# Optimization experiments

Hardware: AMD Instinct MI355X
Metric: run time of the kernel (lower is better)

## Reference

```python
import jax, jax.numpy as jnp
import numpy as np

B, S, E = 2, 2048, 1024
H, BLK = 16, 32
HD = E // H


def setup_inputs() -> dict:
    key = jax.random.key(0)
    ks = jax.random.split(key, 9)
    s = 1.0 / np.sqrt(E)
    return {
        "x": jax.random.normal(ks[0], (B, S, E), dtype=jnp.float32),
        "Wq": jax.random.normal(ks[1], (E, E), dtype=jnp.float32) * s,
        "bq": jnp.zeros((E,), dtype=jnp.float32),
        "Wk": jax.random.normal(ks[2], (E, E), dtype=jnp.float32) * s,
        "bk": jnp.zeros((E,), dtype=jnp.float32),
        "Wv": jax.random.normal(ks[3], (E, E), dtype=jnp.float32) * s,
        "bv": jnp.zeros((E,), dtype=jnp.float32),
        "Wo": jax.random.normal(ks[4], (E, E), dtype=jnp.float32) * s,
        "bo": jnp.zeros((E,), dtype=jnp.float32),
    }


def reference(x, Wq, bq, Wk, bk, Wv, bv, Wo, bo):
    b, s, e = x.shape
    # projections (torch Linear: x @ W.T + b), split heads -> [b, h, s, hd]
    def proj(W, bias):
        return (x @ W.T + bias).reshape(b, s, H, HD).transpose(0, 2, 1, 3)

    q = proj(Wq, bq)
    k = proj(Wk, bk)
    v = proj(Wv, bv)

    scale = 1.0 / np.sqrt(HD)
    scores = jnp.einsum("bhqd,bhkd->bhqk", q, k) * scale  # [b,h,s,s]

    # block-causal mask: query block i attends to all key blocks j <= i
    idx = jnp.arange(s)
    allowed = (idx[None, :] // BLK) <= (idx[:, None] // BLK)  # [s, s]
    scores = jnp.where(allowed[None, None], scores, jnp.float32(-1e9))

    probs = jax.nn.softmax(scores, axis=-1)
    attn = jnp.einsum("bhqk,bhkd->bhqd", probs, v)  # [b,h,s,hd]
    out = attn.transpose(0, 2, 1, 3).reshape(b, s, e)
    return out @ Wo.T + bo
```

## Files before the change

kernel.cpp:

```cpp
#include <hip/hip_runtime.h>
#include <hip/hip_bf16.h>
#include <stdint.h>

#define BATCH 2
#define S_LEN 2048
#define EMB   1024
#define NHEAD 16
#define HDIM  64

typedef __attribute__((ext_vector_type(8)))  __bf16 bf16x8;
typedef __attribute__((ext_vector_type(4)))  __bf16 bf16x4;
typedef __attribute__((ext_vector_type(4)))  float  f32x4;
typedef __attribute__((ext_vector_type(16))) float  f32x16;

#define ZERO16 ((f32x16){0.f,0.f,0.f,0.f,0.f,0.f,0.f,0.f,0.f,0.f,0.f,0.f,0.f,0.f,0.f,0.f})
#define SM_SCALE_LOG2 0.18033688011112042f

static __device__ __forceinline__ void gload_lds16(const void* g, void* l) {
    __builtin_amdgcn_global_load_lds(
        (__attribute__((address_space(1))) void*)g,
        (__attribute__((address_space(3))) void*)l,
        16, 0, 0);
}

__global__ void f2b_all(const float* __restrict__ x,
                        const float* __restrict__ Wq, const float* __restrict__ Wk,
                        const float* __restrict__ Wv, const float* __restrict__ Wo,
                        __bf16* __restrict__ xb,
                        __bf16* __restrict__ wqb, __bf16* __restrict__ wkb,
                        __bf16* __restrict__ wvb, __bf16* __restrict__ wob) {
    int i = blockIdx.x * blockDim.x + threadIdx.x;
    const float* s;
    __bf16* d;
    int off;
    if (i < (1 << 20)) {
        s = x; d = xb; off = i;
    } else {
        int r   = i - (1 << 20);
        int seg = r >> 18;
        off = r & ((1 << 18) - 1);
        s = seg == 0 ? Wq : seg == 1 ? Wk : seg == 2 ? Wv : Wo;
        d = seg == 0 ? wqb : seg == 1 ? wkb : seg == 2 ? wvb : wob;
    }
    float4 v = reinterpret_cast<const float4*>(s)[off];
    bf16x4 o = { (__bf16)v.x, (__bf16)v.y, (__bf16)v.z, (__bf16)v.w };
    reinterpret_cast<bf16x4*>(d)[off] = o;
}

__global__ __launch_bounds__(256)
void gemm_o64(const __bf16* __restrict__ A, const __bf16* __restrict__ W,
              const float* __restrict__ bias, float* __restrict__ out,
              int M, int N, int K) {
    __shared__ __align__(16) __bf16 As[2][128 * 64];
    __shared__ __align__(16) __bf16 Bs[2][64 * 64];

    const int t    = threadIdx.x;
    const int w    = t >> 6;
    const int lane = t & 63;
    const int m0   = blockIdx.y * 128;
    const int n0   = blockIdx.x * 64;
    const int wr   = w * 32;
    const int fr   = lane & 15;
    const int g16  = lane >> 4;

    f32x4 acc[2][4];
#pragma unroll
    for (int i = 0; i < 2; ++i)
#pragma unroll
        for (int n = 0; n < 4; ++n) acc[i][n] = (f32x4){0.f, 0.f, 0.f, 0.f};

    auto stage = [&](int kt, int buf) {
#pragma unroll
        for (int i = 0; i < 4; ++i) {
            int chunk = i * 256 + t;
            int row   = chunk >> 3;
            int col   = ((chunk & 7) ^ (row & 7)) * 8;
            gload_lds16(A + (size_t)(m0 + row) * K + kt + col,
                        (char*)&As[buf][0] + i * 4096 + w * 1024);
        }
#pragma unroll
        for (int i = 0; i < 2; ++i) {
            int chunk = i * 256 + t;
            int row   = chunk >> 3;
            int col   = ((chunk & 7) ^ (row & 7)) * 8;
            gload_lds16(W + (size_t)(n0 + row) * K + kt + col,
                        (char*)&Bs[buf][0] + i * 4096 + w * 1024);
        }
    };

    stage(0, 0);
    __syncthreads();

    const int NK = K / 64;
    for (int k6 = 0; k6 < NK; ++k6) {
        const int cur = k6 & 1;
        if (k6 + 1 < NK) stage((k6 + 1) * 64, cur ^ 1);

#pragma unroll
        for (int kh = 0; kh < 2; ++kh) {
            bf16x8 af[2], bfv[4];
#pragma unroll
            for (int m = 0; m < 2; ++m) {
                int row = wr + m * 16 + fr;
                int cg  = ((4 * kh + g16) ^ (row & 7)) * 8;
                af[m] = *(const bf16x8*)&As[cur][row * 64 + cg];
            }
#pragma unroll
            for (int n = 0; n < 4; ++n) {
                int row = n * 16 + fr;
                int cg  = ((4 * kh + g16) ^ (row & 7)) * 8;
                bfv[n] = *(const bf16x8*)&Bs[cur][row * 64 + cg];
            }
#pragma unroll
            for (int m = 0; m < 2; ++m)
#pragma unroll
                for (int n = 0; n < 4; ++n)
                    acc[m][n] = __builtin_amdgcn_mfma_f32_16x16x32_bf16(
                        af[m], bfv[n], acc[m][n], 0, 0, 0);
        }
        __syncthreads();
    }

    const int rbase = (lane >> 4) * 4;
#pragma unroll
    for (int m = 0; m < 2; ++m) {
#pragma unroll
        for (int n = 0; n < 4; ++n) {
            int col  = n0 + n * 16 + fr;
            float bv = bias[col];
#pragma unroll
            for (int jj = 0; jj < 4; ++jj) {
                int row = m0 + wr + m * 16 + rbase + jj;
                out[(size_t)row * N + col] = acc[m][n][jj] + bv;
            }
        }
    }
}

__global__ __launch_bounds__(512)
void gemm_qkv(const __bf16* __restrict__ xb,
              const __bf16* __restrict__ Wqb, const __bf16* __restrict__ Wkb,
              const __bf16* __restrict__ Wvb,
              const float* __restrict__ bqp, const float* __restrict__ bkp,
              const float* __restrict__ bvp,
              __bf16* __restrict__ Qo, __bf16* __restrict__ Ko,
              __bf16* __restrict__ VTo, int K) {
    __shared__ __align__(16) __bf16 As[2][128 * 64];
    __shared__ __align__(16) __bf16 Bs[2][128 * 64];

    const bool isV = (blockIdx.x >= 8);
    const int  xx  = blockIdx.x & 7;

    const int t    = threadIdx.x;
    const int w    = t >> 6;
    const int lane = t & 63;
    const int wr   = (w >> 2) * 64;
    const int wc   = (w & 3) * 32;
    const int fr   = lane & 15;
    const int g16  = lane >> 4;
    const int rbase = (lane >> 4) * 4;

    auto run_pass = [&](const __bf16* Ap, const __bf16* Wp,
                        const float* bias, __bf16* outp,
                        int m0, int n0, bool vt) {
        f32x4 acc[4][2];
#pragma unroll
        for (int i = 0; i < 4; ++i)
#pragma unroll
            for (int jq = 0; jq < 2; ++jq) acc[i][jq] = (f32x4){0.f, 0.f, 0.f, 0.f};

        auto stage = [&](int kt, int buf) {
#pragma unroll
            for (int i = 0; i < 2; ++i) {
                int chunk = i * 512 + t;
                int row   = chunk >> 3;
                int col   = ((chunk & 7) ^ (row & 7)) * 8;
                gload_lds16(Ap + (size_t)(m0 + row) * K + kt + col,
                            (char*)&As[buf][0] + i * 8192 + w * 1024);
                gload_lds16(Wp + (size_t)(n0 + row) * K + kt + col,
                            (char*)&Bs[buf][0] + i * 8192 + w * 1024);
            }
        };

        stage(0, 0);
        __syncthreads();

        const int NK = K / 64;
        for (int k6 = 0; k6 < NK; ++k6) {
            const int cur = k6 & 1;
            if (k6 + 1 < NK) stage((k6 + 1) * 64, cur ^ 1);

#pragma unroll
            for (int kh = 0; kh < 2; ++kh) {
                bf16x8 af[4], bfv[2];
#pragma unroll
                for (int m = 0; m < 4; ++m) {
                    int row = wr + m * 16 + fr;
                    int cg  = ((4 * kh + g16) ^ (row & 7)) * 8;
                    af[m] = *(const bf16x8*)&As[cur][row * 64 + cg];
                }
#pragma unroll
                for (int n = 0; n < 2; ++n) {
                    int row = wc + n * 16 + fr;
                    int cg  = ((4 * kh + g16) ^ (row & 7)) * 8;
                    bfv[n] = *(const bf16x8*)&Bs[cur][row * 64 + cg];
                }
#pragma unroll
                for (int m = 0; m < 4; ++m)
#pragma unroll
                    for (int n = 0; n < 2; ++n)
                        acc[m][n] = __builtin_amdgcn_mfma_f32_16x16x32_bf16(
                            af[m], bfv[n], acc[m][n], 0, 0, 0);
            }
            __syncthreads();
        }

        if (vt) {
#pragma unroll
            for (int m = 0; m < 4; ++m) {
#pragma unroll
                for (int n = 0; n < 2; ++n) {
                    int col = n0 + wc + n * 16 + fr;
                    int b   = col >> 11, s = col & (S_LEN - 1);
#pragma unroll
                    for (int jj = 0; jj < 4; ++jj) {
                        int row = m0 + wr + m * 16 + rbase + jj;
                        int hh  = row >> 6, d = row & (HDIM - 1);
                        float v = acc[m][n][jj] + bias[row];
                        VTo[(((size_t)(b * NHEAD + hh)) * HDIM + d) * S_LEN + s] =
                            (__bf16)v;
                    }
                }
            }
        } else {
#pragma unroll
            for (int m = 0; m < 4; ++m) {
#pragma unroll
                for (int n = 0; n < 2; ++n) {
                    int col  = n0 + wc + n * 16 + fr;
                    float bv = bias[col];
#pragma unroll
                    for (int jj = 0; jj < 4; ++jj) {
                        int row = m0 + wr + m * 16 + rbase + jj;
                        float v = acc[m][n][jj] + bv;
                        int b = row >> 11, s = row & (S_LEN - 1);
                        int hh = col >> 6, d = col & (HDIM - 1);
                        outp[(((size_t)(b * NHEAD + hh)) * S_LEN + s) * HDIM + d] =
                            (__bf16)v;
                    }
                }
            }
        }
    };

    if (!isV) {
        const int m0 = blockIdx.y * 128;
        const int n0 = xx * 128;
        run_pass(xb, Wqb, bqp, Qo, m0, n0, false);
        run_pass(xb, Wkb, bkp, Ko, m0, n0, false);
    } else {
        run_pass(Wvb, xb, bvp, VTo, xx * 128, blockIdx.y * 128, true);
    }
}

__global__ __launch_bounds__(512, 4)
void attn12_kernel(const __bf16* __restrict__ Q, const __bf16* __restrict__ Kv,
                   const __bf16* __restrict__ VT, __bf16* __restrict__ out) {
    __shared__ __align__(16) char smem[66560];
    __bf16* Kt0 = (__bf16*)smem;
    __bf16* Vt0 = (__bf16*)(smem + 32768);

    const int t    = threadIdx.x;
    const int w8   = t >> 6;
    const int lane = t & 63;
    const int h    = lane >> 5;
    const int q32  = lane & 31;
    const int j    = w8 & 3;
    const int h2   = w8 >> 2;
    const int bh   = blockIdx.x;
    const int yy   = blockIdx.y;
    const int qt   = (yy < 8) ? (15 - yy) : (yy - 8);
    const int qb   = 4 * qt + j;
    const int C    = qt + 1;

    const __bf16* Qp  = Q  + (size_t)bh * S_LEN * HDIM;
    const __bf16* Kp  = Kv + (size_t)bh * S_LEN * HDIM;
    const __bf16* VTp = VT + (size_t)bh * HDIM * S_LEN;

    const int qrow = qb * 32 + q32;

    bf16x8 qreg[4];
#pragma unroll
    for (int ks = 0; ks < 4; ++ks)
        qreg[ks] = *(const bf16x8*)&Qp[(size_t)qrow * HDIM + 16 * ks + 8 * h];

    f32x16 oacc0 = ZERO16, oacc1 = ZERO16;
    float lrun = 0.f;

    {
#pragma unroll
        for (int i = 0; i < 2; ++i) {
            int c16 = i * 512 + t;
            int key = c16 >> 3;
            int d0  = ((c16 & 7) ^ (key & 7)) * 8;
            gload_lds16(Kp + (size_t)key * HDIM + d0, (char*)Kt0 + c16 * 16);
        }
#pragma unroll
        for (int i = 0; i < 2; ++i) {
            int c16 = i * 512 + t;
            int d   = c16 >> 4;
            int o   = c16 & 15;
            gload_lds16(VTp + (size_t)d * S_LEN + ((o ^ (d & 7)) * 8),
                        (char*)Vt0 + c16 * 16);
        }
        __syncthreads();
    }

    for (int c = 0; c < C; ++c) {
        const int cur = c & 1;
        if (c + 1 < C) {
            const int kb = (c + 1) * 128;
#pragma unroll
            for (int i = 0; i < 2; ++i) {
                int c16 = i * 512 + t;
                int key = c16 >> 3;
                int d0  = ((c16 & 7) ^ (key & 7)) * 8;
                gload_lds16(Kp + (size_t)(kb + key) * HDIM + d0,
                            (char*)Kt0 + (cur ^ 1) * 16384 + c16 * 16);
            }
#pragma unroll
            for (int i = 0; i < 2; ++i) {
                int c16 = i * 512 + t;
                int d   = c16 >> 4;
                int o   = c16 & 15;
                gload_lds16(VTp + (size_t)d * S_LEN + kb + ((o ^ (d & 7)) * 8),
                            (char*)Vt0 + (cur ^ 1) * 16384 + c16 * 16);
            }
        }

        const int g0 = 4 * c + 2 * h2;
        const __bf16* Ktc = Kt0 + cur * 8192;
        const __bf16* Vtc = Vt0 + cur * 8192;

#pragma unroll
        for (int u = 0; u < 2; ++u) {
            if (g0 + u > qb) break;
            const int kl = 64 * h2 + 32 * u;

            f32x16 sac = ZERO16;
            __builtin_amdgcn_s_setprio(1);
#pragma unroll
            for (int ks = 0; ks < 4; ++ks) {
                bf16x8 kf = *(const bf16x8*)&Ktc[(kl + q32) * 64 +
                                ((16 * ks + 8 * h) ^ ((q32 & 7) << 3))];
                sac = __builtin_amdgcn_mfma_f32_32x32x16_bf16(kf, qreg[ks], sac, 0, 0, 0);
            }
            __builtin_amdgcn_s_setprio(0);

            float ps = 0.f;
#pragma unroll
            for (int r = 0; r < 16; ++r) {
                float pv = exp2f(sac[r] * SM_SCALE_LOG2);
                ps += pv;
                sac[r] = pv;
            }
            ps += __shfl_xor(ps, 32);
            lrun += ps;

            unsigned L[4], H[4];
#pragma unroll
            for (int g = 0; g < 4; ++g) {
                asm("v_cvt_pk_bf16_f32 %0, %1, %2"
                    : "=v"(L[g]) : "v"(sac[4 * g]), "v"(sac[4 * g + 1]));
                asm("v_cvt_pk_bf16_f32 %0, %1, %2"
                    : "=v"(H[g]) : "v"(sac[4 * g + 2]), "v"(sac[4 * g + 3]));
            }

            __builtin_amdgcn_s_setprio(1);
#pragma unroll
            for (int s2 = 0; s2 < 2; ++s2) {
                unsigned a0 = L[2 * s2], b0 = L[2 * s2 + 1];
                unsigned a1 = H[2 * s2], b1 = H[2 * s2 + 1];
                asm("v_permlane32_swap_b32 %0, %1" : "+v"(a0), "+v"(b0));
                asm("v_permlane32_swap_b32 %0, %1" : "+v"(a1), "+v"(b1));
                unsigned wvw[4] = { a0, a1, b0, b1 };
                bf16x8 pa = *(bf16x8*)wvw;

                const int klb = kl + 16 * s2 + 8 * h;
#pragma unroll
                for (int n = 0; n < 2; ++n) {
                    int d = 32 * n + q32;
                    bf16x8 vf = *(const bf16x8*)&Vtc[d * 128 +
                                    (klb ^ ((d & 7) << 3))];
                    if (n == 0)
                        oacc0 = __builtin_amdgcn_mfma_f32_32x32x16_bf16(pa, vf, oacc0, 0, 0, 0);
                    else
                        oacc1 = __builtin_amdgcn_mfma_f32_32x32x16_bf16(pa, vf, oacc1, 0, 0, 0);
                }
            }
            __builtin_amdgcn_s_setprio(0);
        }

        __syncthreads();
    }

    float* Oex = (float*)smem;
    float* MLl = (float*)(smem + 65536);

    if (h == 0) MLl[w8 * 32 + q32] = lrun;
    if (h2 == 1) {
        float* ob = Oex + j * 2048;
#pragma unroll
        for (int q2 = 0; q2 < 4; ++q2)
#pragma unroll
            for (int jj = 0; jj < 4; ++jj) {
                int r  = 4 * q2 + jj;
                int rl = 8 * q2 + 4 * h + jj;
                ob[rl * 64 + q32]      = oacc0[r];
                ob[rl * 64 + 32 + q32] = oacc1[r];
            }
    }
    __syncthreads();

    if (h2 == 0) {
        const int b = bh >> 4, hh = bh & (NHEAD - 1);
        __bf16* op = out + (size_t)b * S_LEN * EMB + hh * HDIM;
        const float* ob = Oex + j * 2048;
#pragma unroll
        for (int q2 = 0; q2 < 4; ++q2) {
            f32x4 la4 = *(const f32x4*)&MLl[j * 32 + 8 * q2 + 4 * h];
            f32x4 lb4 = *(const f32x4*)&MLl[(j + 4) * 32 + 8 * q2 + 4 * h];
#pragma unroll
            for (int jj = 0; jj < 4; ++jj) {
                float inv = 1.f / (la4[jj] + lb4[jj]);
                int r  = 4 * q2 + jj;
                int rl = 8 * q2 + 4 * h + jj;
                int row = qb * 32 + rl;
                float v0 = (oacc0[r] + ob[rl * 64 + q32]) * inv;
                float v1 = (oacc1[r] + ob[rl * 64 + 32 + q32]) * inv;
                op[(size_t)row * EMB + q32]      = (__bf16)v0;
                op[(size_t)row * EMB + 32 + q32] = (__bf16)v1;
            }
        }
    }
}

extern "C" void kernel_launch(void* const* d_in, const int* in_sizes, int n_in,
                              void* d_out, int out_size, void* d_ws, size_t ws_size,
                              hipStream_t stream) {
    const float* x  = (const float*)d_in[0];
    const float* Wq = (const float*)d_in[1];
    const float* bq = (const float*)d_in[2];
    const float* Wk = (const float*)d_in[3];
    const float* bk = (const float*)d_in[4];
    const float* Wv = (const float*)d_in[5];
    const float* bv = (const float*)d_in[6];
    const float* Wo = (const float*)d_in[7];
    const float* bo = (const float*)d_in[8];
    float* out = (float*)d_out;

    char* ws = (char*)d_ws;
    __bf16* xb  = (__bf16*)(ws + 0);
    __bf16* wqb = (__bf16*)(ws + 8388608);
    __bf16* wkb = (__bf16*)(ws + 10485760);
    __bf16* wvb = (__bf16*)(ws + 12582912);
    __bf16* wob = (__bf16*)(ws + 14680064);
    __bf16* Qb  = (__bf16*)(ws + 16777216);
    __bf16* Kb  = (__bf16*)(ws + 25165824);
    __bf16* VTb = (__bf16*)(ws + 33554432);
    __bf16* Ab  = (__bf16*)(ws + 41943040);

    const int M = BATCH * S_LEN;
    const int N = EMB;
    const int K = EMB;

    f2b_all<<<8192, 256, 0, stream>>>(x, Wq, Wk, Wv, Wo, xb, wqb, wkb, wvb, wob);

    gemm_qkv<<<dim3(16, 32), 512, 0, stream>>>(
        xb, wqb, wkb, wvb, bq, bk, bv, Qb, Kb, VTb, K);

    attn12_kernel<<<dim3(BATCH * NHEAD, 16), 512, 0, stream>>>(Qb, Kb, VTb, Ab);

    gemm_o64<<<dim3(16, M / 128), 256, 0, stream>>>(Ab, wob, bo, out, M, N, K);
}
```

Measured before the change: 104.0 us.

## Split QKV GEMM into independent 128x64 tiles over a 3D grid

Replaces the QKV projection kernel, which had 512-thread blocks with Q/K blocks doing two sequential passes and V blocks doing one, with a 256-thread kernel. Each block now computes a single 128x64 tile for one of Q, K or V, selected by blockIdx.z. This balances work per block and raises the block count from 512 to 1536 to improve occupancy and load balance across CUs. In exchange, the x tile is no longer reused across the Q and K passes, so more global loads are issued per output tile.

```diff
diff --git a/kernel.cpp b/kernel.cpp
--- a/kernel.cpp
+++ b/kernel.cpp
@@ -137,129 +137,138 @@
     }
 }
 
-__global__ __launch_bounds__(512)
-void gemm_qkv(const __bf16* __restrict__ xb,
-              const __bf16* __restrict__ Wqb, const __bf16* __restrict__ Wkb,
-              const __bf16* __restrict__ Wvb,
-              const float* __restrict__ bqp, const float* __restrict__ bkp,
-              const float* __restrict__ bvp,
-              __bf16* __restrict__ Qo, __bf16* __restrict__ Ko,
-              __bf16* __restrict__ VTo, int K) {
+__global__ __launch_bounds__(256)
+void gemm_qkv3(const __bf16* __restrict__ xb,
+               const __bf16* __restrict__ Wqb, const __bf16* __restrict__ Wkb,
+               const __bf16* __restrict__ Wvb,
+               const float* __restrict__ bqp, const float* __restrict__ bkp,
+               const float* __restrict__ bvp,
+               __bf16* __restrict__ Qo, __bf16* __restrict__ Ko,
+               __bf16* __restrict__ VTo, int K) {
     __shared__ __align__(16) __bf16 As[2][128 * 64];
-    __shared__ __align__(16) __bf16 Bs[2][128 * 64];
-
-    const bool isV = (blockIdx.x >= 8);
-    const int  xx  = blockIdx.x & 7;
+    __shared__ __align__(16) __bf16 Bs[2][64 * 64];
+
+    const int z = blockIdx.z;
+
+    const __bf16* Ap;
+    const __bf16* Wp;
+    const float*  bias;
+    int m0, n0;
+    if (z == 2) {
+        int id = blockIdx.y * 16 + blockIdx.x;
+        m0 = (id >> 6) * 128;
+        n0 = (id & 63) * 64;
+        Ap = Wvb; Wp = xb; bias = bvp;
+    } else {
+        m0 = blockIdx.y * 128;
+        n0 = blockIdx.x * 64;
+        Ap = xb;
+        Wp   = (z == 0) ? Wqb : Wkb;
+        bias = (z == 0) ? bqp : bkp;
+    }
 
     const int t    = threadIdx.x;
     const int w    = t >> 6;
     const int lane = t & 63;
-    const int wr   = (w >> 2) * 64;
-    const int wc   = (w & 3) * 32;
+    const int wr   = w * 32;
     const int fr   = lane & 15;
     const int g16  = lane >> 4;
+
+    f32x4 acc[2][4];
+#pragma unroll
+    for (int i = 0; i < 2; ++i)
+#pragma unroll
+        for (int n = 0; n < 4; ++n) acc[i][n] = (f32x4){0.f, 0.f, 0.f, 0.f};
+
+    auto stage = [&](int kt, int buf) {
+#pragma unroll
+        for (int i = 0; i < 4; ++i) {
+            int chunk = i * 256 + t;
+            int row   = chunk >> 3;
+            int col   = ((chunk & 7) ^ (row & 7)) * 8;
+            gload_lds16(Ap + (size_t)(m0 + row) * K + kt + col,
+                        (char*)&As[buf][0] + i * 4096 + w * 1024);
+        }
+#pragma unroll
+        for (int i = 0; i < 2; ++i) {
+            int chunk = i * 256 + t;
+            int row   = chunk >> 3;
+            int col   = ((chunk & 7) ^ (row & 7)) * 8;
+            gload_lds16(Wp + (size_t)(n0 + row) * K + kt + col,
+                        (char*)&Bs[buf][0] + i * 4096 + w * 1024);
+        }
+    };
+
+    stage(0, 0);
+    __syncthreads();
+
+    const int NK = K / 64;
+    for (int k6 = 0; k6 < NK; ++k6) {
+        const int cur = k6 & 1;
+        if (k6 + 1 < NK) stage((k6 + 1) * 64, cur ^ 1);
+
+#pragma unroll
+        for (int kh = 0; kh < 2; ++kh) {
+            bf16x8 af[2], bfv[4];
+#pragma unroll
+            for (int m = 0; m < 2; ++m) {
+                int row = wr + m * 16 + fr;
+                int cg  = ((4 * kh + g16) ^ (row & 7)) * 8;
+                af[m] = *(const bf16x8*)&As[cur][row * 64 + cg];
+            }
+#pragma unroll
+            for (int n = 0; n < 4; ++n) {
+                int row = n * 16 + fr;
+                int cg  = ((4 * kh + g16) ^ (row & 7)) * 8;
+                bfv[n] = *(const bf16x8*)&Bs[cur][row * 64 + cg];
+            }
+#pragma unroll
+            for (int m = 0; m < 2; ++m)
+#pragma unroll
+                for (int n = 0; n < 4; ++n)
+                    acc[m][n] = __builtin_amdgcn_mfma_f32_16x16x32_bf16(
+                        af[m], bfv[n], acc[m][n], 0, 0, 0);
+        }
+        __syncthreads();
+    }
+
     const int rbase = (lane >> 4) * 4;
-
-    auto run_pass = [&](const __bf16* Ap, const __bf16* Wp,
-                        const float* bias, __bf16* outp,
-                        int m0, int n0, bool vt) {
-        f32x4 acc[4][2];
-#pragma unroll
-        for (int i = 0; i < 4; ++i)
-#pragma unroll
-            for (int jq = 0; jq < 2; ++jq) acc[i][jq] = (f32x4){0.f, 0.f, 0.f, 0.f};
-
-        auto stage = [&](int kt, int buf) {
-#pragma unroll
-            for (int i = 0; i < 2; ++i) {
-                int chunk = i * 512 + t;
-                int row   = chunk >> 3;
-                int col   = ((chunk & 7) ^ (row & 7)) * 8;
-                gload_lds16(Ap + (size_t)(m0 + row) * K + kt + col,
-                            (char*)&As[buf][0] + i * 8192 + w * 1024);
-                gload_lds16(Wp + (size_t)(n0 + row) * K + kt + col,
-                            (char*)&Bs[buf][0] + i * 8192 + w * 1024);
-            }
-        };
-
-        stage(0, 0);
-        __syncthreads();
-
-        const int NK = K / 64;
-        for (int k6 = 0; k6 < NK; ++k6) {
-            const int cur = k6 & 1;
-            if (k6 + 1 < NK) stage((k6 + 1) * 64, cur ^ 1);
-
-#pragma unroll
-            for (int kh = 0; kh < 2; ++kh) {
-                bf16x8 af[4], bfv[2];
-#pragma unroll
-                for (int m = 0; m < 4; ++m) {
-                    int row = wr + m * 16 + fr;
-                    int cg  = ((4 * kh + g16) ^ (row & 7)) * 8;
-                    af[m] = *(const bf16x8*)&As[cur][row * 64 + cg];
+    if (z == 2) {
+#pragma unroll
+        for (int m = 0; m < 2; ++m) {
+#pragma unroll
+            for (int n = 0; n < 4; ++n) {
+                int col = n0 + n * 16 + fr;
+                int b   = col >> 11, s = col & (S_LEN - 1);
+#pragma unroll
+                for (int jj = 0; jj < 4; ++jj) {
+                    int row = m0 + wr + m * 16 + rbase + jj;
+                    int hh  = row >> 6, d = row & (HDIM - 1);
+                    float v = acc[m][n][jj] + bias[row];
+                    VTo[(((size_t)(b * NHEAD + hh)) * HDIM + d) * S_LEN + s] =
+                        (__bf16)v;
                 }
-#pragma unroll
-                for (int n = 0; n < 2; ++n) {
-                    int row = wc + n * 16 + fr;
-                    int cg  = ((4 * kh + g16) ^ (row & 7)) * 8;
-                    bfv[n] = *(const bf16x8*)&Bs[cur][row * 64 + cg];
+            }
+        }
+    } else {
+        __bf16* outp = (z == 0) ? Qo : Ko;
+#pragma unroll
+        for (int m = 0; m < 2; ++m) {
+#pragma unroll
+            for (int n = 0; n < 4; ++n) {
+                int col  = n0 + n * 16 + fr;
+                float bv = bias[col];
+#pragma unroll
+                for (int jj = 0; jj < 4; ++jj) {
+                    int row = m0 + wr + m * 16 + rbase + jj;
+                    float v = acc[m][n][jj] + bv;
+                    int b = row >> 11, s = row & (S_LEN - 1);
+                    int hh = col >> 6, d = col & (HDIM - 1);
+                    outp[(((size_t)(b * NHEAD + hh)) * S_LEN + s) * HDIM + d] =
+                        (__bf16)v;
                 }
-#pragma unroll
-                for (int m = 0; m < 4; ++m)
-#pragma unroll
-                    for (int n = 0; n < 2; ++n)
-                        acc[m][n] = __builtin_amdgcn_mfma_f32_16x16x32_bf16(
-                            af[m], bfv[n], acc[m][n], 0, 0, 0);
-            }
-            __syncthreads();
-        }
-
-        if (vt) {
-#pragma unroll
-            for (int m = 0; m < 4; ++m) {
-#pragma unroll
-                for (int n = 0; n < 2; ++n) {
-                    int col = n0 + wc + n * 16 + fr;
-                    int b   = col >> 11, s = col & (S_LEN - 1);
-#pragma unroll
-                    for (int jj = 0; jj < 4; ++jj) {
-                        int row = m0 + wr + m * 16 + rbase + jj;
-                        int hh  = row >> 6, d = row & (HDIM - 1);
-                        float v = acc[m][n][jj] + bias[row];
-                        VTo[(((size_t)(b * NHEAD + hh)) * HDIM + d) * S_LEN + s] =
-                            (__bf16)v;
-                    }
-                }
-            }
-        } else {
-#pragma unroll
-            for (int m = 0; m < 4; ++m) {
-#pragma unroll
-                for (int n = 0; n < 2; ++n) {
-                    int col  = n0 + wc + n * 16 + fr;
-                    float bv = bias[col];
-#pragma unroll
-                    for (int jj = 0; jj < 4; ++jj) {
-                        int row = m0 + wr + m * 16 + rbase + jj;
-                        float v = acc[m][n][jj] + bv;
-                        int b = row >> 11, s = row & (S_LEN - 1);
-                        int hh = col >> 6, d = col & (HDIM - 1);
-                        outp[(((size_t)(b * NHEAD + hh)) * S_LEN + s) * HDIM + d] =
-                            (__bf16)v;
-                    }
-                }
-            }
-        }
-    };
-
-    if (!isV) {
-        const int m0 = blockIdx.y * 128;
-        const int n0 = xx * 128;
-        run_pass(xb, Wqb, bqp, Qo, m0, n0, false);
-        run_pass(xb, Wkb, bkp, Ko, m0, n0, false);
-    } else {
-        run_pass(Wvb, xb, bvp, VTo, xx * 128, blockIdx.y * 128, true);
+            }
+        }
     }
 }
 
@@ -476,7 +485,7 @@
 
     f2b_all<<<8192, 256, 0, stream>>>(x, Wq, Wk, Wv, Wo, xb, wqb, wkb, wvb, wob);
 
-    gemm_qkv<<<dim3(16, 32), 512, 0, stream>>>(
+    gemm_qkv3<<<dim3(16, 32, 3), 256, 0, stream>>>(
         xb, wqb, wkb, wvb, bq, bk, bv, Qb, Kb, VTb, K);
 
     attn12_kernel<<<dim3(BATCH * NHEAD, 16), 512, 0, stream>>>(Qb, Kb, VTb, Ab);
```

New measurement: 102.7 us. Within noise of the previous version (-1.3%).
